# Kernel tuning notes

Measured on AMD Instinct MI355X. Metric: run time of the kernel, lower is better.

The kernel has to match this reference:

```python
import jax, jax.numpy as jnp
import numpy as np

B, S, D = 4, 2048, 1024
H = 16
DK = D // H  # 64

def setup_inputs() -> dict:
    key = jax.random.key(0)
    ks = jax.random.split(key, 5)
    scale = 0.02
    return {
        "x": jax.random.normal(ks[0], (B, S, D), dtype=jnp.float32),
        "Wq": jax.random.normal(ks[1], (D, D), dtype=jnp.float32) * scale,
        "Wk": jax.random.normal(ks[2], (D, D), dtype=jnp.float32) * scale,
        "Wv": jax.random.normal(ks[3], (D, D), dtype=jnp.float32) * scale,
        "Wo": jax.random.normal(ks[4], (D, D), dtype=jnp.float32) * scale,
    }

def reference(x, Wq, Wk, Wv, Wo):
    b, s, d = x.shape
    h, dk = H, DK
    # torch nn.Linear(bias=False): y = x @ W.T
    q = (x @ Wq.T).reshape(b, s, h, dk).transpose(0, 2, 1, 3)  # [b,h,s,dk]
    k = (x @ Wk.T).reshape(b, s, h, dk).transpose(0, 2, 1, 3)
    v = (x @ Wv.T).reshape(b, s, h, dk).transpose(0, 2, 1, 3)
    scores = jnp.einsum('bhqd,bhkd->bhqk', q, k) * (dk ** -0.5)
    causal = jnp.triu(jnp.ones((s, s), dtype=bool), k=1)  # True = masked out
    scores = jnp.where(causal, -jnp.inf, scores)
    probs = jax.nn.softmax(scores, axis=-1)
    attn = jnp.einsum('bhqk,bhkd->bhqd', probs, v)  # [b,h,s,dk]
    attn = attn.transpose(0, 2, 1, 3).reshape(b, s, d)
    return attn @ Wo.T
```

## Files before the change

kernel.cpp:

```cpp
#include <hip/hip_runtime.h>

typedef __attribute__((ext_vector_type(8))) short bf16x8;
typedef __attribute__((ext_vector_type(4))) float f32x4;
typedef unsigned int u32;
typedef unsigned short u16;

constexpr int Bb = 4, S = 2048, D = 1024, H = 16, DK = 64, M = Bb * S;

#if __has_builtin(__builtin_amdgcn_exp2f)
#define EXP2F __builtin_amdgcn_exp2f
#else
#define EXP2F exp2f
#endif

__device__ __forceinline__ u16 f2bf(float f) {
  u32 u = __float_as_uint(f);
  return (u16)((u + 0x7fffu + ((u >> 16) & 1u)) >> 16);
}

__device__ __forceinline__ void gld_lds16(const u16* g, u16* l) {
  __builtin_amdgcn_global_load_lds((const __attribute__((address_space(1))) u32*)g,
                                   (__attribute__((address_space(3))) u32*)l, 16, 0, 0);
}

__global__ void cast_kernel(const float* __restrict__ s, u16* __restrict__ d, int n) {
  int i = (blockIdx.x * blockDim.x + threadIdx.x) * 4;
  if (i >= n) return;
  float4 f = *(const float4*)(s + i);
  ushort4 o;
  o.x = f2bf(f.x); o.y = f2bf(f.y); o.z = f2bf(f.z); o.w = f2bf(f.w);
  *(ushort4*)(d + i) = o;
}

struct CastArgs { const float* s[4]; u16* d[4]; float sc[4]; };
__global__ void cast4_kernel(CastArgs a) {
  int i = (blockIdx.x * blockDim.x + threadIdx.x) * 4;
  int w = i >> 20;
  int off = i & ((1 << 20) - 1);
  float sc = a.sc[w];
  float4 f = *(const float4*)(a.s[w] + off);
  ushort4 o;
  o.x = f2bf(f.x * sc); o.y = f2bf(f.y * sc); o.z = f2bf(f.z * sc); o.w = f2bf(f.w * sc);
  *(ushort4*)(a.d[w] + off) = o;
}

template <bool OUTF32>
__device__ __forceinline__ void gemm_core(const u16* __restrict__ A,
                                          const u16* __restrict__ Bt,
                                          float* __restrict__ Cf, u16* __restrict__ Cb,
                                          int Nn, int Kk, int m0, int n0,
                                          u16* As, u16* Bs) {
  const int tid = threadIdx.x, wave = tid >> 6, lane = tid & 63;
  const int quad = lane >> 4, col = lane & 15;
  const int wm = wave >> 1, wn = wave & 1;

  f32x4 acc[4][4];
#pragma unroll
  for (int i = 0; i < 4; i++)
#pragma unroll
    for (int j = 0; j < 4; j++) acc[i][j] = (f32x4){0.f, 0.f, 0.f, 0.f};

  for (int k0 = 0; k0 < Kk; k0 += 64) {
#pragma unroll
    for (int j = 0; j < 4; j++) {
      int g = (wave * 4 + j) * 64;
      int gl = g + lane;
      int r = gl >> 3, sl = gl & 7;
      int kof = (sl ^ (r & 7)) * 8;
      const u16* ga = A + (size_t)(m0 + r) * Kk + k0 + kof;
      gld_lds16(ga, &As[g * 8]);
      const u16* gb = Bt + (size_t)(n0 + r) * Kk + k0 + kof;
      gld_lds16(gb, &Bs[g * 8]);
    }
    __syncthreads();
#pragma unroll
    for (int kb = 0; kb < 2; kb++) {
      bf16x8 af[4], bfr[4];
#pragma unroll
      for (int mi = 0; mi < 4; mi++) {
        int R = wm * 64 + mi * 16 + col;
        af[mi] = *(const bf16x8*)&As[R * 64 + (((kb * 4 + quad) ^ (R & 7)) << 3)];
      }
#pragma unroll
      for (int ni = 0; ni < 4; ni++) {
        int R = wn * 64 + ni * 16 + col;
        bfr[ni] = *(const bf16x8*)&Bs[R * 64 + (((kb * 4 + quad) ^ (R & 7)) << 3)];
      }
#pragma unroll
      for (int mi = 0; mi < 4; mi++)
#pragma unroll
        for (int ni = 0; ni < 4; ni++)
          acc[mi][ni] = __builtin_amdgcn_mfma_f32_16x16x32_bf16(af[mi], bfr[ni], acc[mi][ni], 0, 0, 0);
    }
    __syncthreads();
  }
#pragma unroll
  for (int mi = 0; mi < 4; mi++)
#pragma unroll
    for (int ni = 0; ni < 4; ni++)
#pragma unroll
      for (int r = 0; r < 4; r++) {
        int row = m0 + wm * 64 + mi * 16 + quad * 4 + r;
        int cc = n0 + wn * 64 + ni * 16 + col;
        float v = acc[mi][ni][r];
        if (OUTF32) Cf[(size_t)row * Nn + cc] = v;
        else Cb[(size_t)row * Nn + cc] = f2bf(v);
      }
}

struct QkvArgs { const u16* bt[3]; u16* c[3]; };
__global__ __launch_bounds__(256) void gemm_qkv(const u16* __restrict__ A, QkvArgs q) {
  __shared__ __align__(16) u16 As[128 * 64];
  __shared__ __align__(16) u16 Bs[128 * 64];
  int sel = blockIdx.x >> 3;
  int n0 = (blockIdx.x & 7) * 128, m0 = blockIdx.y * 128;
  gemm_core<false>(A, q.bt[sel], nullptr, q.c[sel], D, D, m0, n0, As, Bs);
}

__global__ __launch_bounds__(256) void gemm_f32(const u16* __restrict__ A,
                                                const u16* __restrict__ Bt,
                                                float* __restrict__ C) {
  __shared__ __align__(16) u16 As[128 * 64];
  __shared__ __align__(16) u16 Bs[128 * 64];
  gemm_core<true>(A, Bt, C, nullptr, D, D, blockIdx.y * 128, blockIdx.x * 128, As, Bs);
}

__global__ __launch_bounds__(256) void attn_kernel(const u16* __restrict__ Q,
                                                   const u16* __restrict__ K,
                                                   const u16* __restrict__ V,
                                                   u16* __restrict__ O) {
  __shared__ __align__(16) u16 Ks[2][2][64 * 32];
  __shared__ __align__(16) u16 Vt[2][64 * 64];
  __shared__ __align__(16) u16 Pw[4][32 * 64];
  const int tid = threadIdx.x, wave = tid >> 6, lane = tid & 63;
  const int quad = lane >> 4, col = lane & 15;
  const int bh = blockIdx.x, b = bh >> 4, h = bh & 15;
  const int pair = blockIdx.y;
  const size_t base = (size_t)b * S * D + h * DK;

  const int vk0 = (tid & 31) * 2;
  const int vdg = tid >> 5;

  bf16x8 bones;
#pragma unroll
  for (int e = 0; e < 8; e++) bones[e] = (short)0x3F80;

  for (int half = 0; half < 2; half++) {
    const int qb = half ? pair : 15 - pair;
    const int qw = qb * 128 + wave * 32;
    const int nkt = 2 * qb + 2;

    bf16x8 aq[2][2];
#pragma unroll
    for (int mi = 0; mi < 2; mi++)
#pragma unroll
      for (int kb = 0; kb < 2; kb++)
        aq[mi][kb] = *(const bf16x8*)(Q + base + (size_t)(qw + mi * 16 + col) * D + kb * 32 + quad * 8);

    f32x4 ao[2][4], lacc[2];
#pragma unroll
    for (int mi = 0; mi < 2; mi++) {
      lacc[mi] = (f32x4){0.f, 0.f, 0.f, 0.f};
#pragma unroll
      for (int dg = 0; dg < 4; dg++) ao[mi][dg] = (f32x4){0.f, 0.f, 0.f, 0.f};
    }

    bf16x8 vA0, vA1, vB0, vB1;
    {
      const u16* vp = V + base + (size_t)vk0 * D + vdg * 8;
      vA0 = *(const bf16x8*)vp; vA1 = *(const bf16x8*)(vp + D);
    }
    __syncthreads();
    {
      int c = tid, cb = wave * 64;
      const u16* g0 = K + base + (size_t)(c >> 2) * D + (c & 3) * 8;
      gld_lds16(g0, &Ks[0][0][cb * 8]);
      gld_lds16(g0 + 32, &Ks[0][1][cb * 8]);
    }
    auto vstage = [&](int buf, bf16x8 r0, bf16x8 r1) {
      int kgrp = vk0 >> 3, kin = vk0 & 7;
      int perm = (kgrp ^ vdg) & 7;
#pragma unroll
      for (int e = 0; e < 8; e++) {
        u32 val = ((u32)(u16)r0[e]) | ((u32)(u16)r1[e] << 16);
        *(u32*)&Vt[buf][(vdg * 8 + e) * 64 + perm * 8 + kin] = val;
      }
    };
    vstage(0, vA0, vA1);
    {
      const u16* vp = V + base + (size_t)(64 + vk0) * D + vdg * 8;
      vB0 = *(const bf16x8*)vp; vB1 = *(const bf16x8*)(vp + D);
    }

    for (int kt = 0; kt < nkt; kt++) {
      const int bf = kt & 1, nb = bf ^ 1, ph = kt & 1;
      __syncthreads();
      const bool active = (kt * 64 <= qw + 31);
      if (kt + 1 < nkt) {
        {
          int c = tid, cb = wave * 64;
          const u16* g0 = K + base + (size_t)((kt + 1) * 64 + (c >> 2)) * D + (c & 3) * 8;
          gld_lds16(g0, &Ks[nb][0][cb * 8]);
          gld_lds16(g0 + 32, &Ks[nb][1][cb * 8]);
        }
        vstage(nb, ph ? vA0 : vB0, ph ? vA1 : vB1);
        if (kt + 2 < nkt) {
          const u16* vp = V + base + (size_t)((kt + 2) * 64 + vk0) * D + vdg * 8;
          if (ph) { vB0 = *(const bf16x8*)vp; vB1 = *(const bf16x8*)(vp + D); }
          else    { vA0 = *(const bf16x8*)vp; vA1 = *(const bf16x8*)(vp + D); }
        }
      }
      if (!active) continue;
      bf16x8 bk0[4], bk1[4];
#pragma unroll
      for (int n16 = 0; n16 < 4; n16++) {
        bk0[n16] = *(const bf16x8*)&Ks[bf][0][(n16 * 16 + col) * 32 + quad * 8];
        bk1[n16] = *(const bf16x8*)&Ks[bf][1][(n16 * 16 + col) * 32 + quad * 8];
      }
      f32x4 sacc[2][4];
#pragma unroll
      for (int mi = 0; mi < 2; mi++)
#pragma unroll
        for (int n16 = 0; n16 < 4; n16++) sacc[mi][n16] = (f32x4){0.f, 0.f, 0.f, 0.f};
#pragma unroll
      for (int mi = 0; mi < 2; mi++)
#pragma unroll
        for (int n16 = 0; n16 < 4; n16++) {
          sacc[mi][n16] = __builtin_amdgcn_mfma_f32_16x16x32_bf16(aq[mi][0], bk0[n16], sacc[mi][n16], 0, 0, 0);
          sacc[mi][n16] = __builtin_amdgcn_mfma_f32_16x16x32_bf16(aq[mi][1], bk1[n16], sacc[mi][n16], 0, 0, 0);
        }
      const bool full = (kt * 64 + 63) <= qw;
#pragma unroll
      for (int mi = 0; mi < 2; mi++)
#pragma unroll
        for (int r = 0; r < 4; r++) {
          int qloc = mi * 16 + quad * 4 + r;
          int qs = quad << 1;
#pragma unroll
          for (int n16 = 0; n16 < 4; n16++) {
            float p = EXP2F(sacc[mi][n16][r]);
            if (!full) {
              int kg = kt * 64 + n16 * 16 + col;
              p = (kg > qw + qloc) ? 0.f : p;
            }
            int kgl = n16 * 16 + col;
            int perm = ((kgl >> 3) ^ qs) & 7;
            Pw[wave][qloc * 64 + perm * 8 + (kgl & 7)] = (u16)(__float_as_uint(p) >> 16);
          }
        }
      bf16x8 bv[2][4];
#pragma unroll
      for (int kb = 0; kb < 2; kb++)
#pragma unroll
        for (int dg = 0; dg < 4; dg++) {
          int d3 = (dg * 2 + (col >> 3)) & 7;
          bv[kb][dg] = *(const bf16x8*)&Vt[bf][(dg * 16 + col) * 64 + (((kb * 4 + quad) ^ d3) << 3)];
        }
#pragma unroll
      for (int mi = 0; mi < 2; mi++) {
        int qs2 = ((col >> 2) & 3) << 1;
        bf16x8 ap0 = *(const bf16x8*)&Pw[wave][(mi * 16 + col) * 64 + (((quad ^ qs2) & 7) << 3)];
        bf16x8 ap1 = *(const bf16x8*)&Pw[wave][(mi * 16 + col) * 64 + ((((4 + quad) ^ qs2) & 7) << 3)];
#pragma unroll
        for (int dg = 0; dg < 4; dg++) {
          ao[mi][dg] = __builtin_amdgcn_mfma_f32_16x16x32_bf16(ap0, bv[0][dg], ao[mi][dg], 0, 0, 0);
          ao[mi][dg] = __builtin_amdgcn_mfma_f32_16x16x32_bf16(ap1, bv[1][dg], ao[mi][dg], 0, 0, 0);
        }
        lacc[mi] = __builtin_amdgcn_mfma_f32_16x16x32_bf16(ap0, bones, lacc[mi], 0, 0, 0);
        lacc[mi] = __builtin_amdgcn_mfma_f32_16x16x32_bf16(ap1, bones, lacc[mi], 0, 0, 0);
      }
    }
#pragma unroll
    for (int mi = 0; mi < 2; mi++)
#pragma unroll
      for (int r = 0; r < 4; r++) {
        float inv = 1.f / lacc[mi][r];
        int q = qw + mi * 16 + quad * 4 + r;
#pragma unroll
        for (int dg = 0; dg < 4; dg++)
          O[base + (size_t)q * D + dg * 16 + col] = f2bf(ao[mi][dg][r] * inv);
      }
  }
}

extern "C" void kernel_launch(void* const* d_in, const int* in_sizes, int n_in,
                              void* d_out, int out_size, void* d_ws, size_t ws_size,
                              hipStream_t stream) {
  const float* x  = (const float*)d_in[0];
  const float* Wq = (const float*)d_in[1];
  const float* Wk = (const float*)d_in[2];
  const float* Wv = (const float*)d_in[3];
  const float* Wo = (const float*)d_in[4];

  u16* xb  = (u16*)d_ws;
  u16* wqb = xb + (size_t)M * D;
  u16* wkb = wqb + (size_t)D * D;
  u16* wvb = wkb + (size_t)D * D;
  u16* wob = wvb + (size_t)D * D;
  u16* Qb  = wob + (size_t)D * D;
  u16* Kb  = Qb + (size_t)M * D;
  u16* Vb  = Kb + (size_t)M * D;
  u16* Ab  = xb;

  cast_kernel<<<M * D / 1024, 256, 0, stream>>>(x, xb, M * D);
  CastArgs ca;
  ca.s[0] = Wq; ca.s[1] = Wk; ca.s[2] = Wv; ca.s[3] = Wo;
  ca.d[0] = wqb; ca.d[1] = wkb; ca.d[2] = wvb; ca.d[3] = wob;
  ca.sc[0] = 0.18033688011112042f;
  ca.sc[1] = 1.f; ca.sc[2] = 1.f; ca.sc[3] = 1.f;
  cast4_kernel<<<4 * D * D / 1024, 256, 0, stream>>>(ca);

  QkvArgs qa;
  qa.bt[0] = wqb; qa.bt[1] = wkb; qa.bt[2] = wvb;
  qa.c[0] = Qb; qa.c[1] = Kb; qa.c[2] = Vb;
  gemm_qkv<<<dim3(24, M / 128), 256, 0, stream>>>(xb, qa);

  attn_kernel<<<dim3(Bb * H, 8), 256, 0, stream>>>(Qb, Kb, Vb, Ab);

  gemm_f32<<<dim3(D / 128, M / 128), 256, 0, stream>>>(Ab, wob, (float*)d_out);
}
```

Measured before the change: 261.7 us.

## Transpose QK^T MFMA operands and re-swizzle K, V, P LDS layouts

Swaps the A/B operands of the QK^T MFMA so each lane holds four consecutive key scores for one query row. P can then be packed and written to LDS as 8-byte stores instead of scalar 16-bit stores. Adds XOR swizzles to the K tile (applied at the global-to-LDS load and undone on read) and changes the V and P swizzle patterns to reduce LDS bank conflicts. It also wraps the MFMA sections in s_setprio to favour matrix issue. The risk is that swizzle mismatches could break correctness, and setprio may have little effect.

```diff
diff --git a/kernel.cpp b/kernel.cpp
--- a/kernel.cpp
+++ b/kernel.cpp
@@ -2,6 +2,7 @@
 
 typedef __attribute__((ext_vector_type(8))) short bf16x8;
 typedef __attribute__((ext_vector_type(4))) float f32x4;
+typedef __attribute__((ext_vector_type(2))) unsigned int u32x2;
 typedef unsigned int u32;
 typedef unsigned short u16;
 
@@ -145,6 +146,15 @@
 #pragma unroll
   for (int e = 0; e < 8; e++) bones[e] = (short)0x3F80;
 
+  auto kdma = [&](int ktile, int buf) {
+    int c = tid, cb = wave * 64;
+    int kk = c >> 2;
+    int dch = (c & 3) ^ ((kk >> 1) & 3);
+    const u16* g0 = K + base + (size_t)(ktile * 64 + kk) * D + dch * 8;
+    gld_lds16(g0, &Ks[buf][0][cb * 8]);
+    gld_lds16(g0 + 32, &Ks[buf][1][cb * 8]);
+  };
+
   for (int half = 0; half < 2; half++) {
     const int qb = half ? pair : 15 - pair;
     const int qw = qb * 128 + wave * 32;
@@ -171,19 +181,14 @@
       vA0 = *(const bf16x8*)vp; vA1 = *(const bf16x8*)(vp + D);
     }
     __syncthreads();
-    {
-      int c = tid, cb = wave * 64;
-      const u16* g0 = K + base + (size_t)(c >> 2) * D + (c & 3) * 8;
-      gld_lds16(g0, &Ks[0][0][cb * 8]);
-      gld_lds16(g0 + 32, &Ks[0][1][cb * 8]);
-    }
+    kdma(0, 0);
     auto vstage = [&](int buf, bf16x8 r0, bf16x8 r1) {
       int kgrp = vk0 >> 3, kin = vk0 & 7;
-      int perm = (kgrp ^ vdg) & 7;
 #pragma unroll
       for (int e = 0; e < 8; e++) {
         u32 val = ((u32)(u16)r0[e]) | ((u32)(u16)r1[e] << 16);
-        *(u32*)&Vt[buf][(vdg * 8 + e) * 64 + perm * 8 + kin] = val;
+        int slot = (kgrp ^ e) & 7;
+        *(u32*)&Vt[buf][(vdg * 8 + e) * 64 + (slot << 3) + kin] = val;
       }
     };
     vstage(0, vA0, vA1);
@@ -197,12 +202,7 @@
       __syncthreads();
       const bool active = (kt * 64 <= qw + 31);
       if (kt + 1 < nkt) {
-        {
-          int c = tid, cb = wave * 64;
-          const u16* g0 = K + base + (size_t)((kt + 1) * 64 + (c >> 2)) * D + (c & 3) * 8;
-          gld_lds16(g0, &Ks[nb][0][cb * 8]);
-          gld_lds16(g0 + 32, &Ks[nb][1][cb * 8]);
-        }
+        kdma(kt + 1, nb);
         vstage(nb, ph ? vA0 : vB0, ph ? vA1 : vB1);
         if (kt + 2 < nkt) {
           const u16* vp = V + base + (size_t)((kt + 2) * 64 + vk0) * D + vdg * 8;
@@ -212,55 +212,64 @@
       }
       if (!active) continue;
       bf16x8 bk0[4], bk1[4];
+      const int ksl = ((quad ^ ((col >> 1) & 3)) & 3) << 3;
 #pragma unroll
       for (int n16 = 0; n16 < 4; n16++) {
-        bk0[n16] = *(const bf16x8*)&Ks[bf][0][(n16 * 16 + col) * 32 + quad * 8];
-        bk1[n16] = *(const bf16x8*)&Ks[bf][1][(n16 * 16 + col) * 32 + quad * 8];
+        bk0[n16] = *(const bf16x8*)&Ks[bf][0][(n16 * 16 + col) * 32 + ksl];
+        bk1[n16] = *(const bf16x8*)&Ks[bf][1][(n16 * 16 + col) * 32 + ksl];
       }
       f32x4 sacc[2][4];
 #pragma unroll
-      for (int mi = 0; mi < 2; mi++)
-#pragma unroll
-        for (int n16 = 0; n16 < 4; n16++) sacc[mi][n16] = (f32x4){0.f, 0.f, 0.f, 0.f};
-#pragma unroll
-      for (int mi = 0; mi < 2; mi++)
+      for (int qi = 0; qi < 2; qi++)
+#pragma unroll
+        for (int n16 = 0; n16 < 4; n16++) sacc[qi][n16] = (f32x4){0.f, 0.f, 0.f, 0.f};
+      __builtin_amdgcn_s_setprio(1);
+#pragma unroll
+      for (int qi = 0; qi < 2; qi++)
 #pragma unroll
         for (int n16 = 0; n16 < 4; n16++) {
-          sacc[mi][n16] = __builtin_amdgcn_mfma_f32_16x16x32_bf16(aq[mi][0], bk0[n16], sacc[mi][n16], 0, 0, 0);
-          sacc[mi][n16] = __builtin_amdgcn_mfma_f32_16x16x32_bf16(aq[mi][1], bk1[n16], sacc[mi][n16], 0, 0, 0);
+          sacc[qi][n16] = __builtin_amdgcn_mfma_f32_16x16x32_bf16(bk0[n16], aq[qi][0], sacc[qi][n16], 0, 0, 0);
+          sacc[qi][n16] = __builtin_amdgcn_mfma_f32_16x16x32_bf16(bk1[n16], aq[qi][1], sacc[qi][n16], 0, 0, 0);
         }
+      __builtin_amdgcn_s_setprio(0);
       const bool full = (kt * 64 + 63) <= qw;
 #pragma unroll
-      for (int mi = 0; mi < 2; mi++)
-#pragma unroll
-        for (int r = 0; r < 4; r++) {
-          int qloc = mi * 16 + quad * 4 + r;
-          int qs = quad << 1;
-#pragma unroll
-          for (int n16 = 0; n16 < 4; n16++) {
-            float p = EXP2F(sacc[mi][n16][r]);
-            if (!full) {
-              int kg = kt * 64 + n16 * 16 + col;
-              p = (kg > qw + qloc) ? 0.f : p;
-            }
-            int kgl = n16 * 16 + col;
-            int perm = ((kgl >> 3) ^ qs) & 7;
-            Pw[wave][qloc * 64 + perm * 8 + (kgl & 7)] = (u16)(__float_as_uint(p) >> 16);
+      for (int qi = 0; qi < 2; qi++) {
+        const int row = qi * 16 + col;
+        const int rsw = row & 7;
+        const int qg = qw + row;
+#pragma unroll
+        for (int n16 = 0; n16 < 4; n16++) {
+          float p0 = EXP2F(sacc[qi][n16][0]);
+          float p1 = EXP2F(sacc[qi][n16][1]);
+          float p2 = EXP2F(sacc[qi][n16][2]);
+          float p3 = EXP2F(sacc[qi][n16][3]);
+          if (!full) {
+            int kg = kt * 64 + n16 * 16 + quad * 4;
+            p0 = (kg + 0 > qg) ? 0.f : p0;
+            p1 = (kg + 1 > qg) ? 0.f : p1;
+            p2 = (kg + 2 > qg) ? 0.f : p2;
+            p3 = (kg + 3 > qg) ? 0.f : p3;
           }
+          u32 lo = (__float_as_uint(p0) >> 16) | (__float_as_uint(p1) & 0xFFFF0000u);
+          u32 hi = (__float_as_uint(p2) >> 16) | (__float_as_uint(p3) & 0xFFFF0000u);
+          int slot = ((n16 * 2 + (quad >> 1)) ^ rsw) & 7;
+          *(u32x2*)&Pw[wave][row * 64 + (slot << 3) + ((quad & 1) << 2)] = (u32x2){lo, hi};
         }
+      }
       bf16x8 bv[2][4];
 #pragma unroll
       for (int kb = 0; kb < 2; kb++)
 #pragma unroll
-        for (int dg = 0; dg < 4; dg++) {
-          int d3 = (dg * 2 + (col >> 3)) & 7;
-          bv[kb][dg] = *(const bf16x8*)&Vt[bf][(dg * 16 + col) * 64 + (((kb * 4 + quad) ^ d3) << 3)];
-        }
+        for (int dg = 0; dg < 4; dg++)
+          bv[kb][dg] = *(const bf16x8*)&Vt[bf][(dg * 16 + col) * 64 + ((((kb * 4 + quad) ^ (col & 7)) & 7) << 3)];
 #pragma unroll
       for (int mi = 0; mi < 2; mi++) {
-        int qs2 = ((col >> 2) & 3) << 1;
-        bf16x8 ap0 = *(const bf16x8*)&Pw[wave][(mi * 16 + col) * 64 + (((quad ^ qs2) & 7) << 3)];
-        bf16x8 ap1 = *(const bf16x8*)&Pw[wave][(mi * 16 + col) * 64 + ((((4 + quad) ^ qs2) & 7) << 3)];
+        const int row = mi * 16 + col;
+        const int rsw = row & 7;
+        bf16x8 ap0 = *(const bf16x8*)&Pw[wave][row * 64 + (((quad ^ rsw) & 7) << 3)];
+        bf16x8 ap1 = *(const bf16x8*)&Pw[wave][row * 64 + ((((4 + quad) ^ rsw) & 7) << 3)];
+        __builtin_amdgcn_s_setprio(1);
 #pragma unroll
         for (int dg = 0; dg < 4; dg++) {
           ao[mi][dg] = __builtin_amdgcn_mfma_f32_16x16x32_bf16(ap0, bv[0][dg], ao[mi][dg], 0, 0, 0);
@@ -268,6 +277,7 @@
         }
         lacc[mi] = __builtin_amdgcn_mfma_f32_16x16x32_bf16(ap0, bones, lacc[mi], 0, 0, 0);
         lacc[mi] = __builtin_amdgcn_mfma_f32_16x16x32_bf16(ap1, bones, lacc[mi], 0, 0, 0);
+        __builtin_amdgcn_s_setprio(0);
       }
     }
 #pragma unroll
```

After: 263.4 us. About the same (+0.6%).
